# Kernel optimization log

Measured on AMD Instinct MI355X. Metric: run time of the kernel, lower is better.

The kernel has to match this reference:

```python
import jax, jax.numpy as jnp
import numpy as np
from itertools import product

NUM_LEVELS = 4
NUM_FEATURES = 4
B, L = 32, 512

def build_kernel(num_features, num_levels):
    # signatory.all_words ordering: words grouped by length 1..num_levels, lexicographic within length
    words = [w for m in range(1, num_levels + 1) for w in product(range(num_features), repeat=m)]
    num_components = num_levels * (num_levels + 1) // 2
    k = np.zeros((num_components, num_features, len(words)), dtype=np.float32)
    for i, word in enumerate(words):
        m = len(word)
        start = m * (m - 1) // 2
        for j, axis in enumerate(word):
            k[start + j, axis, i] = 1.0
    return jnp.asarray(k)

def setup_inputs() -> dict:
    key = jax.random.key(0)
    x = jax.random.normal(key, (B, L, NUM_FEATURES), dtype=jnp.float32)
    return {"x": x, "kernel": build_kernel(NUM_FEATURES, NUM_LEVELS)}

def reference(x, kernel):
    Bn, Ln, F = x.shape
    NF = kernel.shape[-1]  # num_functionals = 340
    # path increments
    seq = x[:, 1:, :] - x[:, :-1, :]                      # (B, L-1, F)
    # lift: (C, B, L-1, NF), C = num_levels*(num_levels+1)/2 = 10
    M = jnp.einsum('blf,cfk->cblk', seq, kernel)
    # level-by-level recursion with independent weights, return_sequences=True
    # then summed over the stacked level axis (stack+sum == running sum of Y terms)
    sig = jnp.cumsum(M[0], axis=1)                        # level 1
    k = 1
    for m in range(1, NUM_LEVELS):
        R = M[k]; k += 1
        for _ in range(m):
            # tf.cumsum(..., exclusive=True) == inclusive cumsum minus self
            R = M[k] * (jnp.cumsum(R, axis=1) - R)
            k += 1
        sig = sig + jnp.cumsum(R, axis=1)
    # prepend zero time step -> (B, L, NF)
    sig = jnp.concatenate([jnp.zeros((Bn, 1, NF), dtype=x.dtype), sig], axis=1)
    # prepend constant-1 functional channel -> (B, L, NF+1)
    return jnp.concatenate([jnp.ones((Bn, Ln, 1), dtype=x.dtype), sig], axis=-1)
```

## Files before the change

kernel.cpp:

```cpp
#include <hip/hip_runtime.h>


#define SIG_B 32
#define SIG_L 512
#define SIG_NSTEP 511
#define SIG_ROW 341
#define SIG_CS 32
#define SIG_C 16
#define SIG_PAD 344

__global__ __launch_bounds__(256) void sigA(const float* __restrict__ x,
                                            float* __restrict__ Lsig) {
    const int bc = blockIdx.x;
    const int b = bc / SIG_C, c = bc % SIG_C;
    const int tid = threadIdx.x;
    const int t0 = c * SIG_CS;
    const int nt = min(SIG_CS, SIG_NSTEP - t0);

    __shared__ float dlds[SIG_CS * 4];
    const float* xb = x + ((size_t)b * SIG_L + t0) * 4;
    if (tid < nt) {
        float4 x0 = *(const float4*)(xb + tid * 4);
        float4 x1 = *(const float4*)(xb + (tid + 1) * 4);
        *(float4*)(dlds + tid * 4) =
            make_float4(x1.x - x0.x, x1.y - x0.y, x1.z - x0.z, x1.w - x0.w);
    }
    __syncthreads();

    const int a = tid >> 6, bb = (tid >> 4) & 3, cc = (tid >> 2) & 3, ee = tid & 3;
    float s1 = 0.f, s2 = 0.f, s3 = 0.f, s4 = 0.f;
    const float* dp = dlds;
    for (int t = 0; t < nt; ++t) {
        const float da = dp[a], db = dp[bb], dc = dp[cc], de = dp[ee];
        dp += 4;
        s4 = fmaf(s3, de, s4);
        s3 = fmaf(s2, dc, s3);
        s2 = fmaf(s1, db, s2);
        s1 += da;
    }
    float* Lr = Lsig + (size_t)bc * SIG_PAD;
    if ((tid & 63) == 0) Lr[1 + a] = s1;
    if ((tid & 15) == 0) Lr[5 + (tid >> 4)] = s2;
    if ((tid & 3) == 0)  Lr[21 + (tid >> 2)] = s3;
    Lr[85 + tid] = s4;
}

__global__ __launch_bounds__(256) void sigC(const float* __restrict__ x,
                                            const float* __restrict__ Lsig,
                                            float* __restrict__ out) {
    const int bc = blockIdx.x;
    const int b = bc / SIG_C, c = bc % SIG_C;
    const int tid = threadIdx.x;
    const int t0 = c * SIG_CS;
    const int nt = min(SIG_CS, SIG_NSTEP - t0);

    __shared__ float dlds[SIG_CS * 4];
    __shared__ float L[(SIG_C - 1) * SIG_PAD];

    const float* xb = x + ((size_t)b * SIG_L + t0) * 4;
    if (tid < SIG_CS) {
        float4 d = make_float4(0.f, 0.f, 0.f, 0.f);
        if (tid < nt) {
            float4 x0 = *(const float4*)(xb + tid * 4);
            float4 x1 = *(const float4*)(xb + (tid + 1) * 4);
            d = make_float4(x1.x - x0.x, x1.y - x0.y, x1.z - x0.z, x1.w - x0.w);
        }
        *(float4*)(dlds + tid * 4) = d;
    }
    {
        const float4* Lb4 = (const float4*)(Lsig + (size_t)b * SIG_C * SIG_PAD);
        float4* L4p = (float4*)L;
        const int nzero = c * (SIG_PAD / 4);
        const int n4 = (SIG_C - 1) * (SIG_PAD / 4);
        for (int i = tid; i < n4; i += 256) {
            float4 v = Lb4[i];
            if (i >= nzero) v = make_float4(0.f, 0.f, 0.f, 0.f);
            L4p[i] = v;
        }
    }
    __syncthreads();

    const int a = tid >> 6, bb = (tid >> 4) & 3, cc = (tid >> 2) & 3, ee = tid & 3;

    float p1 = 0.f, p2 = 0.f, p3 = 0.f, p4 = 0.f;
#pragma unroll
    for (int j = 0; j < SIG_C - 1; ++j) {
        const float* Lc = L + j * SIG_PAD;
        const float l1a = Lc[1 + a], l1b = Lc[1 + bb], l1c = Lc[1 + cc], l1e = Lc[1 + ee];
        const float l2ab = Lc[5 + 4 * a + bb], l2bc = Lc[5 + 4 * bb + cc],
                    l2ce = Lc[5 + 4 * cc + ee];
        const float l3abc = Lc[21 + 16 * a + 4 * bb + cc],
                    l3bce = Lc[21 + 16 * bb + 4 * cc + ee];
        const float l4 = Lc[85 + tid];
        p4 += p3 * l1e + p2 * l2ce + p1 * l3bce + l4;
        p3 += p2 * l1c + p1 * l2bc + l3abc;
        p2 += p1 * l1b + l2ab;
        p1 += l1a;
    }

    float* row = out + ((size_t)b * SIG_L + (t0 + 1)) * SIG_ROW;

    if (c == 0) {
        float* r0 = out + (size_t)b * SIG_L * SIG_ROW;
        if (tid == 0)        __builtin_nontemporal_store(1.0f, r0 + 0);
        if ((tid & 63) == 0) __builtin_nontemporal_store(0.f, r0 + 1 + a);
        if ((tid & 15) == 0) __builtin_nontemporal_store(0.f, r0 + 5 + (tid >> 4));
        if ((tid & 3) == 0)  __builtin_nontemporal_store(0.f, r0 + 21 + (tid >> 2));
        __builtin_nontemporal_store(0.f, r0 + 85 + tid);
    }

    for (int tb = 0; tb < SIG_CS; tb += 4) {
        float o1_0, o2_0, o3_0, o4_0, o1_1, o2_1, o3_1, o4_1;
        float o1_2, o2_2, o3_2, o4_2, o1_3, o2_3, o3_3, o4_3;
#define SIG_STEP_SNAP(U, O1, O2, O3, O4)                                     \
        do {                                                                 \
            const float* dp_ = dlds + (tb + (U)) * 4;                        \
            const float da_ = dp_[a], db_ = dp_[bb],                         \
                        dc_ = dp_[cc], de_ = dp_[ee];                        \
            p4 = fmaf(p3, de_, p4);             \
            p3 = fmaf(p2, dc_, p3);                                          \
            p2 = fmaf(p1, db_, p2);                                          \
            p1 += da_;                                                       \
            O1 = p1; O2 = p2; O3 = p3; O4 = p4;                              \
        } while (0)
        SIG_STEP_SNAP(0, o1_0, o2_0, o3_0, o4_0);
        SIG_STEP_SNAP(1, o1_1, o2_1, o3_1, o4_1);
        SIG_STEP_SNAP(2, o1_2, o2_2, o3_2, o4_2);
        SIG_STEP_SNAP(3, o1_3, o2_3, o3_3, o4_3);
#undef SIG_STEP_SNAP

#define SIG_STORE_ROW(U, O1, O2, O3, O4)                                     \
        do {                                                                 \
            if (tb + (U) < nt) {                                             \
                float* r_ = row + (size_t)(tb + (U)) * SIG_ROW;              \
                if (tid == 0)                                                \
                    __builtin_nontemporal_store(1.0f, r_ + 0);               \
                if ((tid & 63) == 0)                                         \
                    __builtin_nontemporal_store(O1, r_ + 1 + a);             \
                if ((tid & 15) == 0)                                         \
                    __builtin_nontemporal_store(O2, r_ + 5 + (tid >> 4));    \
                if ((tid & 3) == 0)                                          \
                    __builtin_nontemporal_store(O3, r_ + 21 + (tid >> 2));   \
                __builtin_nontemporal_store(O4, r_ + 85 + tid);              \
            }                                                                \
        } while (0)
        SIG_STORE_ROW(0, o1_0, o2_0, o3_0, o4_0);
        SIG_STORE_ROW(1, o1_1, o2_1, o3_1, o4_1);
        SIG_STORE_ROW(2, o1_2, o2_2, o3_2, o4_2);
        SIG_STORE_ROW(3, o1_3, o2_3, o3_3, o4_3);
#undef SIG_STORE_ROW
    }
}

extern "C" void kernel_launch(void* const* d_in, const int* in_sizes, int n_in,
                              void* d_out, int out_size, void* d_ws, size_t ws_size,
                              hipStream_t stream) {
    const float* x = (const float*)d_in[0];
    float* out = (float*)d_out;
    float* Lsig = (float*)d_ws;

    sigA<<<SIG_B * SIG_C, 256, 0, stream>>>(x, Lsig);
    sigC<<<SIG_B * SIG_C, 256, 0, stream>>>(x, Lsig, out);
}
```

Baseline: 20.61 us.

## Split sigA chunk scan across warps and merge with Chen combine

sigA previously ran a serial 32-step recurrence per thread over the whole chunk. Now each of the four wavefronts scans an 8-step sub-chunk, with each thread covering four first-index words. The per-wavefront partial signatures go to shared memory and wave 0 merges them with Chen's identity. This shortens the serial dependency chain in sigA, at the cost of an extra barrier, shared-memory traffic and a combine step done by a single wavefront.

```diff
diff --git a/kernel.cpp b/kernel.cpp
--- a/kernel.cpp
+++ b/kernel.cpp
@@ -8,41 +8,112 @@
 #define SIG_CS 32
 #define SIG_C 16
 #define SIG_PAD 344
+#define SIG_WS 8
 
 __global__ __launch_bounds__(256) void sigA(const float* __restrict__ x,
                                             float* __restrict__ Lsig) {
     const int bc = blockIdx.x;
     const int b = bc / SIG_C, c = bc % SIG_C;
     const int tid = threadIdx.x;
+    const int w = tid >> 6, l = tid & 63;
     const int t0 = c * SIG_CS;
     const int nt = min(SIG_CS, SIG_NSTEP - t0);
 
     __shared__ float dlds[SIG_CS * 4];
+    __shared__ float S[4 * SIG_PAD];
+
     const float* xb = x + ((size_t)b * SIG_L + t0) * 4;
-    if (tid < nt) {
-        float4 x0 = *(const float4*)(xb + tid * 4);
-        float4 x1 = *(const float4*)(xb + (tid + 1) * 4);
-        *(float4*)(dlds + tid * 4) =
-            make_float4(x1.x - x0.x, x1.y - x0.y, x1.z - x0.z, x1.w - x0.w);
+    if (tid < SIG_CS) {
+        float4 d = make_float4(0.f, 0.f, 0.f, 0.f);
+        if (tid < nt) {
+            float4 x0 = *(const float4*)(xb + tid * 4);
+            float4 x1 = *(const float4*)(xb + (tid + 1) * 4);
+            d = make_float4(x1.x - x0.x, x1.y - x0.y, x1.z - x0.z, x1.w - x0.w);
+        }
+        *(float4*)(dlds + tid * 4) = d;
     }
     __syncthreads();
 
-    const int a = tid >> 6, bb = (tid >> 4) & 3, cc = (tid >> 2) & 3, ee = tid & 3;
-    float s1 = 0.f, s2 = 0.f, s3 = 0.f, s4 = 0.f;
-    const float* dp = dlds;
-    for (int t = 0; t < nt; ++t) {
-        const float da = dp[a], db = dp[bb], dc = dp[cc], de = dp[ee];
+    const int b2 = (l >> 4) & 3, cc = (l >> 2) & 3, ee = l & 3;
+
+    float s1_0 = 0.f, s2_0 = 0.f, s3_0 = 0.f, s4_0 = 0.f;
+    float s1_1 = 0.f, s2_1 = 0.f, s3_1 = 0.f, s4_1 = 0.f;
+    float s1_2 = 0.f, s2_2 = 0.f, s3_2 = 0.f, s4_2 = 0.f;
+    float s1_3 = 0.f, s2_3 = 0.f, s3_3 = 0.f, s4_3 = 0.f;
+
+    const float* dp = dlds + w * SIG_WS * 4;
+#pragma unroll
+    for (int u = 0; u < SIG_WS; ++u) {
+        const float d0 = dp[0], d1 = dp[1], d2 = dp[2], d3 = dp[3];
+        const float db = dp[b2], dcv = dp[cc], de = dp[ee];
         dp += 4;
-        s4 = fmaf(s3, de, s4);
-        s3 = fmaf(s2, dc, s3);
-        s2 = fmaf(s1, db, s2);
-        s1 += da;
-    }
-    float* Lr = Lsig + (size_t)bc * SIG_PAD;
-    if ((tid & 63) == 0) Lr[1 + a] = s1;
-    if ((tid & 15) == 0) Lr[5 + (tid >> 4)] = s2;
-    if ((tid & 3) == 0)  Lr[21 + (tid >> 2)] = s3;
-    Lr[85 + tid] = s4;
+        s4_0 = fmaf(s3_0, de, s4_0); s3_0 = fmaf(s2_0, dcv, s3_0);
+        s2_0 = fmaf(s1_0, db, s2_0); s1_0 += d0;
+        s4_1 = fmaf(s3_1, de, s4_1); s3_1 = fmaf(s2_1, dcv, s3_1);
+        s2_1 = fmaf(s1_1, db, s2_1); s1_1 += d1;
+        s4_2 = fmaf(s3_2, de, s4_2); s3_2 = fmaf(s2_2, dcv, s3_2);
+        s2_2 = fmaf(s1_2, db, s2_2); s1_2 += d2;
+        s4_3 = fmaf(s3_3, de, s4_3); s3_3 = fmaf(s2_3, dcv, s3_3);
+        s2_3 = fmaf(s1_3, db, s2_3); s1_3 += d3;
+    }
+
+    {
+        float* Sw = S + w * SIG_PAD;
+        if (l == 0) { Sw[1] = s1_0; Sw[2] = s1_1; Sw[3] = s1_2; Sw[4] = s1_3; }
+        if ((l & 15) == 0) {
+            Sw[5 + b2] = s2_0;  Sw[5 + 4 + b2] = s2_1;
+            Sw[5 + 8 + b2] = s2_2; Sw[5 + 12 + b2] = s2_3;
+        }
+        if ((l & 3) == 0) {
+            Sw[21 + (l >> 2)] = s3_0;      Sw[21 + 16 + (l >> 2)] = s3_1;
+            Sw[21 + 32 + (l >> 2)] = s3_2; Sw[21 + 48 + (l >> 2)] = s3_3;
+        }
+        Sw[85 + l] = s4_0;       Sw[85 + 64 + l] = s4_1;
+        Sw[85 + 128 + l] = s4_2; Sw[85 + 192 + l] = s4_3;
+    }
+    __syncthreads();
+
+    if (w == 0) {
+        float p1_0 = 0.f, p2_0 = 0.f, p3_0 = 0.f, p4_0 = 0.f;
+        float p1_1 = 0.f, p2_1 = 0.f, p3_1 = 0.f, p4_1 = 0.f;
+        float p1_2 = 0.f, p2_2 = 0.f, p3_2 = 0.f, p4_2 = 0.f;
+        float p1_3 = 0.f, p2_3 = 0.f, p3_3 = 0.f, p4_3 = 0.f;
+#pragma unroll
+        for (int j = 0; j < 4; ++j) {
+            const float* Sc = S + j * SIG_PAD;
+            const float l1b = Sc[1 + b2], l1c = Sc[1 + cc], l1e = Sc[1 + ee];
+            const float l2bc = Sc[5 + 4 * b2 + cc], l2ce = Sc[5 + 4 * cc + ee];
+            const float l3bce = Sc[21 + 16 * b2 + 4 * cc + ee];
+            const float l1a0 = Sc[1], l1a1 = Sc[2], l1a2 = Sc[3], l1a3 = Sc[4];
+#define SIG_COMB(A, P1, P2, P3, P4, L1A)                                     \
+            do {                                                             \
+                const float l2ab = Sc[5 + 4 * (A) + b2];                     \
+                const float l3abc = Sc[21 + 16 * (A) + 4 * b2 + cc];         \
+                const float l4 = Sc[85 + 64 * (A) + l];                      \
+                P4 += P3 * l1e + P2 * l2ce + P1 * l3bce + l4;                \
+                P3 += P2 * l1c + P1 * l2bc + l3abc;                          \
+                P2 += P1 * l1b + l2ab;                                       \
+                P1 += L1A;                                                   \
+            } while (0)
+            SIG_COMB(0, p1_0, p2_0, p3_0, p4_0, l1a0);
+            SIG_COMB(1, p1_1, p2_1, p3_1, p4_1, l1a1);
+            SIG_COMB(2, p1_2, p2_2, p3_2, p4_2, l1a2);
+            SIG_COMB(3, p1_3, p2_3, p3_3, p4_3, l1a3);
+#undef SIG_COMB
+        }
+        float* Lr = Lsig + (size_t)bc * SIG_PAD;
+        if (l == 0) { Lr[1] = p1_0; Lr[2] = p1_1; Lr[3] = p1_2; Lr[4] = p1_3; }
+        if ((l & 15) == 0) {
+            Lr[5 + b2] = p2_0;  Lr[5 + 4 + b2] = p2_1;
+            Lr[5 + 8 + b2] = p2_2; Lr[5 + 12 + b2] = p2_3;
+        }
+        if ((l & 3) == 0) {
+            Lr[21 + (l >> 2)] = p3_0;      Lr[21 + 16 + (l >> 2)] = p3_1;
+            Lr[21 + 32 + (l >> 2)] = p3_2; Lr[21 + 48 + (l >> 2)] = p3_3;
+        }
+        Lr[85 + l] = p4_0;       Lr[85 + 64 + l] = p4_1;
+        Lr[85 + 128 + l] = p4_2; Lr[85 + 192 + l] = p4_3;
+    }
 }
 
 __global__ __launch_bounds__(256) void sigC(const float* __restrict__ x,
```

New measurement: 20.70 us. Within noise of the previous version (+0.4%).
